# Kernel optimization log

Hardware: AMD Instinct MI355X
Metric: run time of the kernel (lower is better)

The kernel has to match this reference:

```python
import jax, jax.numpy as jnp
import numpy as np

# irreps_in == irreps_out == 512x0e + 256x1o + 128x2e
# each entry: (multiplicity, irrep dimension 2l+1)
IRREPS = [(512, 1), (256, 3), (128, 5)]
DIM_TOTAL = sum(m * d for m, d in IRREPS)          # 1920
WEIGHT_NUMEL = sum(m * m for m, _ in IRREPS)       # 344064
N = 16384


def setup_inputs() -> dict:
    key = jax.random.key(0)
    kx, kw = jax.random.split(key)
    x = jax.random.normal(kx, (N, DIM_TOTAL), dtype=jnp.float32)
    weight = jax.random.normal(kw, (WEIGHT_NUMEL,), dtype=jnp.float32)
    return {"x": x, "weight": weight}


def reference(x, weight):
    """Segmented (block-diagonal per irrep) linear mixing with 1/sqrt(fan_in) norm."""
    n = x.shape[0]
    outs = []
    x_off = 0
    w_off = 0
    for mul, d in IRREPS:
        seg = x[:, x_off:x_off + mul * d].reshape(n, mul, d)      # [N, mul, 2l+1]
        W = weight[w_off:w_off + mul * mul].reshape(mul, mul)     # [mul_in, mul_out]
        scale = jnp.asarray(1.0 / np.sqrt(mul), dtype=x.dtype)
        y = jnp.einsum('nui,uv->nvi', seg, W) * scale             # channel mix per component
        outs.append(y.reshape(n, mul * d))
        x_off += mul * d
        w_off += mul * mul
    return jnp.concatenate(outs, axis=-1)
```

## Files before the change

### kernel.cpp

```cpp
#include <hip/hip_runtime.h>
#include <hip/hip_bf16.h>


typedef float  f32x4  __attribute__((ext_vector_type(4)));
typedef short  bf16x8 __attribute__((ext_vector_type(8)));

#define ROWLEN 1920

__device__ __forceinline__ unsigned short f2bf(float f) {
    union { float f; unsigned int u; } c; c.f = f;
    unsigned int u = c.u;
    u += 0x7fffu + ((u >> 16) & 1u);
    return (unsigned short)(u >> 16);
}

__global__ __launch_bounds__(256) void prep_weights(const float* __restrict__ w,
                                                    unsigned short* __restrict__ wt) {
    int g = blockIdx.x * 256 + threadIdx.x;
    if (g >= 344064) return;
    int base, sh;
    if      (g < 262144) { base = 0;      sh = 9; }
    else if (g < 327680) { base = 262144; sh = 8; }
    else                 { base = 327680; sh = 7; }
    int local = g - base;
    int u = local >> sh;
    int v = local & ((1 << sh) - 1);
    wt[base + (v << sh) + u] = f2bf(w[g]);
}

template<int MUL, int D, int TN, int X_OFF, int WT_BASE>
__global__ __launch_bounds__(256) void seg_gemm(const float* __restrict__ x,
                                                const unsigned short* __restrict__ wt,
                                                float* __restrict__ out,
                                                float scale) {
    constexpr int KB      = 32;
    constexpr int NSTEP   = MUL / KB;
    constexpr int M_LOG   = TN * D;
    constexpr int MT      = M_LOG / 16;
    constexpr int WAVE_NT = MUL / 64;
    constexpr int STRIDE  = KB + 8;
    constexpr int ROW_F   = KB * D;
    constexpr int ROW_F4  = ROW_F / 4;
    constexpr int TOT_F4  = TN * ROW_F4;

    __shared__ unsigned short lds[M_LOG * STRIDE];

    const int tid  = threadIdx.x;
    const int wave = tid >> 6;
    const int lane = tid & 63;
    const int q    = lane >> 4;
    const int t16  = lane & 15;
    const int n0   = blockIdx.x * TN;

    f32x4 acc[MT][WAVE_NT];
#pragma unroll
    for (int a = 0; a < MT; ++a)
#pragma unroll
        for (int b = 0; b < WAVE_NT; ++b) acc[a][b] = (f32x4)0.0f;

    const float* __restrict__ xblk = x + X_OFF + n0 * ROWLEN;
    const unsigned short* __restrict__ wblk = wt + WT_BASE;
    const int vbase = wave * (WAVE_NT * 16) + t16;

    for (int ks = 0; ks < NSTEP; ++ks) {
        const int u0 = ks * KB;
        __syncthreads();
        for (int idx = tid; idx < TOT_F4; idx += 256) {
            const int nl = idx / ROW_F4;
            const int c4 = (idx % ROW_F4) * 4;
            const f32x4 vv = *(const f32x4*)(xblk + nl * ROWLEN + u0 * D + c4);
            if (D == 1) {
                unsigned int lo = f2bf(vv[0]) | ((unsigned int)f2bf(vv[1]) << 16);
                unsigned int hi = f2bf(vv[2]) | ((unsigned int)f2bf(vv[3]) << 16);
                unsigned int* p = (unsigned int*)&lds[nl * STRIDE + c4];
                p[0] = lo; p[1] = hi;
            } else {
#pragma unroll
                for (int e = 0; e < 4; ++e) {
                    const int c = c4 + e;
                    const int u = c / D;
                    const int i = c % D;
                    lds[(i * TN + nl) * STRIDE + u] = f2bf(vv[e]);
                }
            }
        }
        __syncthreads();
        bf16x8 afr[MT];
#pragma unroll
        for (int tm = 0; tm < MT; ++tm)
            afr[tm] = *(const bf16x8*)&lds[(16 * tm + t16) * STRIDE + q * 8];
#pragma unroll
        for (int tv = 0; tv < WAVE_NT; ++tv) {
            const bf16x8 bfr = *(const bf16x8*)&wblk[(vbase + tv * 16) * MUL + u0 + q * 8];
#pragma unroll
            for (int tm = 0; tm < MT; ++tm)
                acc[tm][tv] = __builtin_amdgcn_mfma_f32_16x16x32_bf16(afr[tm], bfr, acc[tm][tv], 0, 0, 0);
        }
    }

#pragma unroll
    for (int tm = 0; tm < MT; ++tm) {
#pragma unroll
        for (int tv = 0; tv < WAVE_NT; ++tv) {
            const int v = vbase + tv * 16;
#pragma unroll
            for (int r = 0; r < 4; ++r) {
                const int rit = q * 4 + r;
                const int nl   = (D == 1) ? (16 * tm + rit) : rit;
                const int comp = (D == 1) ? 0 : tm;
                out[(n0 + nl) * ROWLEN + X_OFF + v * D + comp] = acc[tm][tv][r] * scale;
            }
        }
    }
}

extern "C" void kernel_launch(void* const* d_in, const int* in_sizes, int n_in,
                              void* d_out, int out_size, void* d_ws, size_t ws_size,
                              hipStream_t stream) {
    const float* x = (const float*)d_in[0];
    const float* w = (const float*)d_in[1];
    float* out = (float*)d_out;
    unsigned short* wt = (unsigned short*)d_ws;

    hipLaunchKernelGGL(prep_weights, dim3((344064 + 255) / 256), dim3(256), 0, stream, w, wt);

    hipLaunchKernelGGL((seg_gemm<512, 1, 32, 0, 0>),
                       dim3(16384 / 32), dim3(256), 0, stream, x, wt, out, 0.044194173824f);
    hipLaunchKernelGGL((seg_gemm<256, 3, 16, 512, 262144>),
                       dim3(16384 / 16), dim3(256), 0, stream, x, wt, out, 0.0625f);
    hipLaunchKernelGGL((seg_gemm<128, 5, 16, 1280, 327680>),
                       dim3(16384 / 16), dim3(256), 0, stream, x, wt, out, 0.088388347648f);
}
```

Baseline: 292.7 us.

## Fuse three segment GEMMs into one launch with whole-K LDS staging

Merges the three per-irrep GEMM kernels into a single kernel that dispatches blocks to segments by block index, interleaving the segments across the grid. Each block now loads its full K extent of x into dynamic LDS (about 33 KB) once, converting it to bf16, instead of reloading per 32-wide K step with two barriers each. The output row mapping is generalized accordingly. This removes per-step synchronization and two launch overheads, at the cost of larger LDS use per block, which may limit occupancy, and no overlap between loads and MFMA.

```diff
diff --git a/kernel.cpp b/kernel.cpp
--- a/kernel.cpp
+++ b/kernel.cpp
@@ -1,5 +1,4 @@
 #include <hip/hip_runtime.h>
-#include <hip/hip_bf16.h>
 
 
 typedef float  f32x4  __attribute__((ext_vector_type(4)));
@@ -29,28 +28,51 @@
 }
 
 template<int MUL, int D, int TN, int X_OFF, int WT_BASE>
-__global__ __launch_bounds__(256) void seg_gemm(const float* __restrict__ x,
-                                                const unsigned short* __restrict__ wt,
-                                                float* __restrict__ out,
-                                                float scale) {
+__device__ __forceinline__ void seg_body(const int bid,
+                                         const float* __restrict__ x,
+                                         const unsigned short* __restrict__ wt,
+                                         float* __restrict__ out,
+                                         const float scale,
+                                         unsigned short* lds) {
     constexpr int KB      = 32;
     constexpr int NSTEP   = MUL / KB;
     constexpr int M_LOG   = TN * D;
     constexpr int MT      = M_LOG / 16;
     constexpr int WAVE_NT = MUL / 64;
-    constexpr int STRIDE  = KB + 8;
-    constexpr int ROW_F   = KB * D;
-    constexpr int ROW_F4  = ROW_F / 4;
-    constexpr int TOT_F4  = TN * ROW_F4;
-
-    __shared__ unsigned short lds[M_LOG * STRIDE];
+    constexpr int ST      = MUL + 8;
+    constexpr int ROW_F4  = MUL * D / 4;
+    constexpr int ITERS   = TN * ROW_F4 / 256;
 
     const int tid  = threadIdx.x;
     const int wave = tid >> 6;
     const int lane = tid & 63;
     const int q    = lane >> 4;
     const int t16  = lane & 15;
-    const int n0   = blockIdx.x * TN;
+    const int n0   = bid * TN;
+
+    const float* __restrict__ xblk = x + X_OFF + n0 * ROWLEN;
+
+#pragma unroll 4
+    for (int it = 0; it < ITERS; ++it) {
+        const int idx = tid + it * 256;
+        const int nl  = idx / ROW_F4;
+        const int c4  = (idx - nl * ROW_F4) * 4;
+        const f32x4 vv = *(const f32x4*)(xblk + nl * ROWLEN + c4);
+        if (D == 1) {
+            unsigned int lo = (unsigned int)f2bf(vv[0]) | ((unsigned int)f2bf(vv[1]) << 16);
+            unsigned int hi = (unsigned int)f2bf(vv[2]) | ((unsigned int)f2bf(vv[3]) << 16);
+            unsigned int* p = (unsigned int*)&lds[nl * ST + c4];
+            p[0] = lo; p[1] = hi;
+        } else {
+#pragma unroll
+            for (int e = 0; e < 4; ++e) {
+                const int c = c4 + e;
+                const int u = c / D;
+                const int i = c - u * D;
+                lds[(i * TN + nl) * ST + u] = f2bf(vv[e]);
+            }
+        }
+    }
 
     f32x4 acc[MT][WAVE_NT];
 #pragma unroll
@@ -58,40 +80,20 @@
 #pragma unroll
         for (int b = 0; b < WAVE_NT; ++b) acc[a][b] = (f32x4)0.0f;
 
-    const float* __restrict__ xblk = x + X_OFF + n0 * ROWLEN;
+    __syncthreads();
+
     const unsigned short* __restrict__ wblk = wt + WT_BASE;
     const int vbase = wave * (WAVE_NT * 16) + t16;
 
+#pragma unroll 1
     for (int ks = 0; ks < NSTEP; ++ks) {
-        const int u0 = ks * KB;
-        __syncthreads();
-        for (int idx = tid; idx < TOT_F4; idx += 256) {
-            const int nl = idx / ROW_F4;
-            const int c4 = (idx % ROW_F4) * 4;
-            const f32x4 vv = *(const f32x4*)(xblk + nl * ROWLEN + u0 * D + c4);
-            if (D == 1) {
-                unsigned int lo = f2bf(vv[0]) | ((unsigned int)f2bf(vv[1]) << 16);
-                unsigned int hi = f2bf(vv[2]) | ((unsigned int)f2bf(vv[3]) << 16);
-                unsigned int* p = (unsigned int*)&lds[nl * STRIDE + c4];
-                p[0] = lo; p[1] = hi;
-            } else {
-#pragma unroll
-                for (int e = 0; e < 4; ++e) {
-                    const int c = c4 + e;
-                    const int u = c / D;
-                    const int i = c % D;
-                    lds[(i * TN + nl) * STRIDE + u] = f2bf(vv[e]);
-                }
-            }
-        }
-        __syncthreads();
         bf16x8 afr[MT];
 #pragma unroll
         for (int tm = 0; tm < MT; ++tm)
-            afr[tm] = *(const bf16x8*)&lds[(16 * tm + t16) * STRIDE + q * 8];
+            afr[tm] = *(const bf16x8*)&lds[(16 * tm + t16) * ST + ks * KB + q * 8];
 #pragma unroll
         for (int tv = 0; tv < WAVE_NT; ++tv) {
-            const bf16x8 bfr = *(const bf16x8*)&wblk[(vbase + tv * 16) * MUL + u0 + q * 8];
+            const bf16x8 bfr = *(const bf16x8*)&wblk[(vbase + tv * 16) * MUL + ks * KB + q * 8];
 #pragma unroll
             for (int tm = 0; tm < MT; ++tm)
                 acc[tm][tv] = __builtin_amdgcn_mfma_f32_16x16x32_bf16(afr[tm], bfr, acc[tm][tv], 0, 0, 0);
@@ -105,12 +107,29 @@
             const int v = vbase + tv * 16;
 #pragma unroll
             for (int r = 0; r < 4; ++r) {
-                const int rit = q * 4 + r;
-                const int nl   = (D == 1) ? (16 * tm + rit) : rit;
-                const int comp = (D == 1) ? 0 : tm;
-                out[(n0 + nl) * ROWLEN + X_OFF + v * D + comp] = acc[tm][tv][r] * scale;
+                const int rit  = q * 4 + r;
+                const int lrow = 16 * tm + rit;
+                const int i    = lrow / TN;
+                const int nl   = lrow - i * TN;
+                out[(n0 + nl) * ROWLEN + X_OFF + v * D + i] = acc[tm][tv][r] * scale;
             }
         }
+    }
+}
+
+__global__ __launch_bounds__(256, 4) void fused_gemm(const float* __restrict__ x,
+                                                     const unsigned short* __restrict__ wt,
+                                                     float* __restrict__ out) {
+    extern __shared__ unsigned short lds[];
+    const int b = blockIdx.x;
+    const int g = b / 5;
+    const int r = b - g * 5;
+    if (r == 0) {
+        seg_body<512, 1, 32, 0, 0>(g, x, wt, out, 0.044194173824f, lds);
+    } else if (r <= 2) {
+        seg_body<256, 3, 16, 512, 262144>(g * 2 + (r - 1), x, wt, out, 0.0625f, lds);
+    } else {
+        seg_body<128, 5, 16, 1280, 327680>(g * 2 + (r - 3), x, wt, out, 0.088388347648f, lds);
     }
 }
 
@@ -123,11 +142,5 @@
     unsigned short* wt = (unsigned short*)d_ws;
 
     hipLaunchKernelGGL(prep_weights, dim3((344064 + 255) / 256), dim3(256), 0, stream, w, wt);
-
-    hipLaunchKernelGGL((seg_gemm<512, 1, 32, 0, 0>),
-                       dim3(16384 / 32), dim3(256), 0, stream, x, wt, out, 0.044194173824f);
-    hipLaunchKernelGGL((seg_gemm<256, 3, 16, 512, 262144>),
-                       dim3(16384 / 16), dim3(256), 0, stream, x, wt, out, 0.0625f);
-    hipLaunchKernelGGL((seg_gemm<128, 5, 16, 1280, 327680>),
-                       dim3(16384 / 16), dim3(256), 0, stream, x, wt, out, 0.088388347648f);
+    hipLaunchKernelGGL(fused_gemm, dim3(2560), dim3(256), 33280, stream, x, wt, out);
 }
```

Result: faster. 283.7 us (-3.1%).
